# Kernel optimization log

Measured on AMD Instinct MI355X. Metric: run time of the kernel, lower is better.

The kernel has to match this reference:

```python
import jax, jax.numpy as jnp
import numpy as np
import math

IN_DIM = 1024
L = 4096
D_MODEL = 512
D_INNER = 1024   # expand=2 * d_model
D_STATE = 16
D_CONV = 4
DT_RANK = 32     # ceil(d_model / 16)
N_LAYERS = 2
RATE = 10


def setup_inputs() -> dict:
    key = jax.random.key(0)
    ks = iter(jax.random.split(key, 32))
    def w(shape, fan_in):
        return jax.random.normal(next(ks), shape, jnp.float32) * (1.0 / math.sqrt(fan_in))
    return {
        "x": jax.random.normal(next(ks), (1, L, IN_DIM), jnp.float32),
        "rate": RATE,
        "fc1_w": w((D_MODEL, IN_DIM), IN_DIM),
        "fc1_b": jnp.zeros((D_MODEL,), jnp.float32),
        "ln_w": jnp.ones((N_LAYERS, D_MODEL), jnp.float32),
        "ln_b": jnp.zeros((N_LAYERS, D_MODEL), jnp.float32),
        "in_proj_w": w((N_LAYERS, 2 * D_INNER, D_MODEL), D_MODEL),
        "conv_w": w((N_LAYERS, D_INNER, D_CONV), D_CONV),
        "conv_b": jnp.zeros((N_LAYERS, D_INNER), jnp.float32),
        "x_proj_w": w((N_LAYERS, DT_RANK + 2 * D_STATE, D_INNER), D_INNER),
        "dt_proj_w": w((N_LAYERS, D_INNER, DT_RANK), DT_RANK),
        "dt_proj_b": jax.random.normal(next(ks), (N_LAYERS, D_INNER), jnp.float32) * 0.1,
        "A_log": jnp.tile(jnp.log(jnp.arange(1, D_STATE + 1, dtype=jnp.float32)), (N_LAYERS, D_INNER, 1)),
        "D_skip": jnp.ones((N_LAYERS, D_INNER), jnp.float32),
        "out_proj_w": w((N_LAYERS, D_MODEL, D_INNER), D_INNER),
        "norm_w": jnp.ones((D_MODEL,), jnp.float32),
        "norm_b": jnp.zeros((D_MODEL,), jnp.float32),
        "attn_w1": w((128, D_MODEL), D_MODEL),
        "attn_b1": jnp.zeros((128,), jnp.float32),
        "attn_w2": w((1, 128), 128),
        "attn_b2": jnp.zeros((1,), jnp.float32),
        "out2048_w": w((2048, D_MODEL), D_MODEL),
        "out2048_b": jnp.zeros((2048,), jnp.float32),
    }


def _layernorm(x, w, b, eps=1e-5):
    mu = x.mean(-1, keepdims=True)
    var = ((x - mu) ** 2).mean(-1, keepdims=True)
    return (x - mu) * jax.lax.rsqrt(var + eps) * w + b


def _causal_conv(x, w, b):
    # depthwise causal conv: x [L, d], w [d, K] -> y[t, d] = sum_k w[d, k] * x[t - (K-1) + k, d]
    K = w.shape[1]
    xp = jnp.pad(x, ((K - 1, 0), (0, 0)))
    y = sum(xp[k:k + x.shape[0]] * w[:, k] for k in range(K))
    return y + b


def _selective_scan(u, dt, A, B, C, Dp, z):
    # u, dt, z: [L, d]; A: [d, n]; B, C: [L, n]; Dp: [d]
    def step(h, inp):
        dt_t, B_t, C_t, u_t = inp
        dA = jnp.exp(dt_t[:, None] * A)                    # [d, n]
        h = dA * h + (dt_t * u_t)[:, None] * B_t[None, :]  # [d, n]
        return h, h @ C_t                                  # y_t: [d]
    h0 = jnp.zeros((u.shape[1], A.shape[1]), u.dtype)
    _, y = jax.lax.scan(step, h0, (dt, B, C, u))
    return (y + u * Dp) * jax.nn.silu(z)


def _srmamba(h, perm, inv, in_w, cw, cb, xw, dtw, dtb, A_log, Dp, ow):
    xz = h @ in_w.T                         # [L, 2*d_inner]
    x, z = jnp.split(xz, 2, axis=-1)
    x, z = x[perm], z[perm]                 # sequence reordering (stride `rate`)
    x = jax.nn.silu(_causal_conv(x, cw, cb))
    dbl = x @ xw.T                          # [L, dt_rank + 2n]
    dt = jax.nn.softplus(dbl[:, :DT_RANK] @ dtw.T + dtb)
    B = dbl[:, DT_RANK:DT_RANK + D_STATE]
    C = dbl[:, DT_RANK + D_STATE:]
    y = _selective_scan(x, dt, -jnp.exp(A_log), B, C, Dp, z)
    return y[inv] @ ow.T                    # restore original order, out_proj


def reference(x, rate, fc1_w, fc1_b, ln_w, ln_b, in_proj_w, conv_w, conv_b, x_proj_w, dt_proj_w, dt_proj_b, A_log, D_skip, out_proj_w, norm_w, norm_b, attn_w1, attn_b1, attn_w2, attn_b2, out2048_w, out2048_b):
    h = jax.nn.relu(x[0] @ fc1_w.T + fc1_b)   # [L, 512]
    Lx = h.shape[0]
    perm = jnp.concatenate([jnp.arange(i, Lx, rate) for i in range(rate)])
    inv = jnp.argsort(perm)
    for l in range(N_LAYERS):
        h = h + _srmamba(_layernorm(h, ln_w[l], ln_b[l]), perm, inv,
                         in_proj_w[l], conv_w[l], conv_b[l], x_proj_w[l],
                         dt_proj_w[l], dt_proj_b[l], A_log[l], D_skip[l], out_proj_w[l])
    h = _layernorm(h, norm_w, norm_b)
    a = jnp.tanh(h @ attn_w1.T + attn_b1) @ attn_w2.T + attn_b2  # [L, 1]
    Aatt = jax.nn.softmax(a[:, 0])                                # [L]
    pooled = Aatt @ h                                             # [512]
    out = pooled @ out2048_w.T + out2048_b                        # [2048]
    return out[None, :], Aatt[None, None, :]
```

## Files before the change

### kernel.cpp

```cpp
#include <hip/hip_runtime.h>
#include <hip/hip_fp16.h>
#include <math.h>

#define L 4096
#define DIN 1024
#define DM 512
#define DI 1024
#define DS 16
#define DTR 32
#define NCH 128
#define CHK 32

typedef _Float16 v8h __attribute__((ext_vector_type(8)));
typedef float v4f __attribute__((ext_vector_type(4)));

__global__ void perm_k(int* __restrict__ perm, const int* __restrict__ ratep) {
    int p = blockIdx.x * blockDim.x + threadIdx.x;
    if (p >= L) return;
    int rate = ratep[0];
    int cum = 0;
    for (int g = 0; g < rate; ++g) {
        int sz = (L - g + rate - 1) / rate;
        if (p < cum + sz) { perm[p] = g + rate * (p - cum); return; }
        cum += sz;
    }
}

__global__ __launch_bounds__(256) void f2h_multi_k(
    const float* __restrict__ s0, _Float16* __restrict__ d0, int b0,
    const float* __restrict__ s1, _Float16* __restrict__ d1, int b1,
    const float* __restrict__ s2, _Float16* __restrict__ d2, int b2,
    const float* __restrict__ s3, _Float16* __restrict__ d3, int b3)
{
    int b = blockIdx.x;
    const float* src; _Float16* dst; int lb;
    if (b < b0)                { src = s0; dst = d0; lb = b; }
    else if (b < b0 + b1)      { src = s1; dst = d1; lb = b - b0; }
    else if (b < b0 + b1 + b2) { src = s2; dst = d2; lb = b - b0 - b1; }
    else                       { src = s3; dst = d3; lb = b - b0 - b1 - b2; }
    int i = (lb * 256 + threadIdx.x) * 4;
    float4 v = *(const float4*)(src + i);
    _Float16 h4[4] = {(_Float16)v.x, (_Float16)v.y, (_Float16)v.z, (_Float16)v.w};
    *(uint2*)(dst + i) = *(uint2*)h4;
}

template<int ACT, int BNT, int HALF>
__global__ __launch_bounds__(256) void hgemm_nt(
    const _Float16* __restrict__ A, int lda,
    const _Float16* __restrict__ B, int ldb,
    void* __restrict__ Cv, int ldc,
    const float* __restrict__ bias, int K, int accum)
{
    constexpr int MI = (BNT == 128) ? 4 : 2;
    __shared__ _Float16 As[128][40];
    __shared__ _Float16 Bs[BNT][40];
    int tid = threadIdx.x;
    int m0 = blockIdx.y * 128, n0 = blockIdx.x * BNT;
    int lane = tid & 63, wave = tid >> 6;
    int wm, wn;
    if constexpr (BNT == 128) { wm = (wave >> 1) * 64; wn = (wave & 1) * 64; }
    else                      { wm = wave * 32;        wn = 0; }
    int quad = lane >> 4, r16 = lane & 15;
    v4f acc[MI][4] = {};

    int srow = tid >> 1;
    int scol = (tid & 1) * 16;
    const _Float16* Ag = A + (size_t)(m0 + srow) * lda + scol;
    int srowB = (BNT == 128) ? srow : (tid >> 2);
    int scolB = (BNT == 128) ? scol : (tid & 3) * 8;
    const _Float16* Bg = B + (size_t)(n0 + srowB) * ldb + scolB;

    uint4 a0, a1, b0, b1;
    a0 = *(const uint4*)(Ag);
    a1 = *(const uint4*)(Ag + 8);
    b0 = *(const uint4*)(Bg);
    if constexpr (BNT == 128) b1 = *(const uint4*)(Bg + 8);

    int KS = K / 32;
    for (int ks = 0; ks < KS; ++ks) {
        __syncthreads();
        *(uint4*)&As[srow][scol] = a0;
        *(uint4*)&As[srow][scol + 8] = a1;
        *(uint4*)&Bs[srowB][scolB] = b0;
        if constexpr (BNT == 128) *(uint4*)&Bs[srowB][scolB + 8] = b1;
        __syncthreads();
        if (ks + 1 < KS) {
            int k0 = (ks + 1) * 32;
            a0 = *(const uint4*)(Ag + k0);
            a1 = *(const uint4*)(Ag + k0 + 8);
            b0 = *(const uint4*)(Bg + k0);
            if constexpr (BNT == 128) b1 = *(const uint4*)(Bg + k0 + 8);
        }
        v8h af[MI], bf[4];
#pragma unroll
        for (int i = 0; i < MI; ++i)
            af[i] = *(const v8h*)&As[wm + i * 16 + r16][quad * 8];
#pragma unroll
        for (int j = 0; j < 4; ++j)
            bf[j] = *(const v8h*)&Bs[wn + j * 16 + r16][quad * 8];
#pragma unroll
        for (int i = 0; i < MI; ++i)
#pragma unroll
            for (int j = 0; j < 4; ++j)
                acc[i][j] = __builtin_amdgcn_mfma_f32_16x16x32_f16(
                    af[i], bf[j], acc[i][j], 0, 0, 0);
    }

#pragma unroll
    for (int i = 0; i < MI; ++i) {
#pragma unroll
        for (int j = 0; j < 4; ++j) {
            int col = n0 + wn + j * 16 + r16;
            int rbase = m0 + wm + i * 16 + quad * 4;
            float bv = bias ? bias[col] : 0.f;
#pragma unroll
            for (int r = 0; r < 4; ++r) {
                float v = acc[i][j][r] + bv;
                if (ACT == 1) v = fmaxf(v, 0.f);
                if constexpr (HALF) {
                    ((_Float16*)Cv)[(size_t)(rbase + r) * ldc + col] = (_Float16)v;
                } else {
                    float* p = (float*)Cv + (size_t)(rbase + r) * ldc + col;
                    if (accum) v += *p;
                    *p = v;
                }
            }
        }
    }
}

#define BM 64
#define BN 64
#define BKK 32
template<int ACT>
__global__ __launch_bounds__(256) void gemm_nt(
    const float* __restrict__ A, int lda,
    const float* __restrict__ B, int ldb,
    float* __restrict__ C, int ldc,
    const float* __restrict__ bias,
    int M, int N, int K, int kchunk, int accum,
    const float* __restrict__ w2, float* __restrict__ avec)
{
    __shared__ float As[BKK][BM + 4];
    __shared__ float Bs[BKK][BN + 4];
    int tid = threadIdx.x;
    int m0 = blockIdx.y * BM;
    int n0 = blockIdx.x * BN;
    int tx = tid & 15, ty = tid >> 4;
    float acc[4][4] = {};
    int arow = tid >> 3;
    int ak = (tid & 7) * 4;
    int kb = blockIdx.z * kchunk;
    int ke = min(K, kb + kchunk);

    for (int k0 = kb; k0 < ke; k0 += BKK) {
#pragma unroll
        for (int r = 0; r < 2; ++r) {
            int row = arow + r * 32;
            float4 va = *(const float4*)(A + (size_t)(m0 + row) * lda + k0 + ak);
            As[ak + 0][row] = va.x; As[ak + 1][row] = va.y;
            As[ak + 2][row] = va.z; As[ak + 3][row] = va.w;
            float4 vb = *(const float4*)(B + (size_t)(n0 + row) * ldb + k0 + ak);
            Bs[ak + 0][row] = vb.x; Bs[ak + 1][row] = vb.y;
            Bs[ak + 2][row] = vb.z; Bs[ak + 3][row] = vb.w;
        }
        __syncthreads();
#pragma unroll
        for (int kk = 0; kk < BKK; ++kk) {
            float4 a4 = *(const float4*)&As[kk][ty * 4];
            float4 b4 = *(const float4*)&Bs[kk][tx * 4];
            float a[4] = {a4.x, a4.y, a4.z, a4.w};
            float b[4] = {b4.x, b4.y, b4.z, b4.w};
#pragma unroll
            for (int i = 0; i < 4; ++i)
#pragma unroll
                for (int j = 0; j < 4; ++j)
                    acc[i][j] = fmaf(a[i], b[j], acc[i][j]);
        }
        __syncthreads();
    }

#pragma unroll
    for (int i = 0; i < 4; ++i) {
        int row = m0 + ty * 4 + i;
        int col = n0 + tx * 4;
        if (ACT == 4) {
            float part = 0.f;
#pragma unroll
            for (int j = 0; j < 4; ++j) {
                float xv = tanhf(acc[i][j] + bias[col + j]);
                part = fmaf(xv, w2[col + j], part);
            }
            atomicAdd(&avec[row], part);
            continue;
        }
        float* cp = C + (size_t)row * ldc + col;
        if (accum == 2) {
#pragma unroll
            for (int j = 0; j < 4; ++j) atomicAdd(cp + j, acc[i][j]);
            continue;
        }
#pragma unroll
        for (int j = 0; j < 4; ++j)
            cp[j] = acc[i][j] + (bias ? bias[col + j] : 0.f);
    }
}

__global__ __launch_bounds__(256) void layernorm_k(
    const float* __restrict__ x, const float* __restrict__ w,
    const float* __restrict__ b, float* __restrict__ o,
    _Float16* __restrict__ oh, float* __restrict__ avec,
    const float* __restrict__ b2)
{
    int row = blockIdx.x;
    int tid = threadIdx.x;
    const float* xr = x + (size_t)row * DM;
    float v0 = xr[tid], v1 = xr[tid + 256];
    float s = v0 + v1, ss = v0 * v0 + v1 * v1;
    for (int off = 32; off; off >>= 1) {
        s += __shfl_down(s, off, 64);
        ss += __shfl_down(ss, off, 64);
    }
    __shared__ float sm[4], sm2[4];
    int wave = tid >> 6, lane = tid & 63;
    if (lane == 0) { sm[wave] = s; sm2[wave] = ss; }
    __syncthreads();
    float tot = sm[0] + sm[1] + sm[2] + sm[3];
    float tot2 = sm2[0] + sm2[1] + sm2[2] + sm2[3];
    float mu = tot * (1.f / DM);
    float var = tot2 * (1.f / DM) - mu * mu;
    float rs = rsqrtf(var + 1e-5f);
    float y0 = (v0 - mu) * rs * w[tid] + b[tid];
    float y1 = (v1 - mu) * rs * w[tid + 256] + b[tid + 256];
    o[(size_t)row * DM + tid] = y0;
    o[(size_t)row * DM + tid + 256] = y1;
    if (oh) {
        oh[(size_t)row * DM + tid] = (_Float16)y0;
        oh[(size_t)row * DM + tid + 256] = (_Float16)y1;
    }
    if (avec && tid == 0) avec[row] = b2[0];
}

__global__ __launch_bounds__(256) void conv_silu_k(
    const _Float16* __restrict__ xz, const int* __restrict__ perm,
    const float* __restrict__ cw, const float* __restrict__ cb,
    float* __restrict__ xc, float* __restrict__ dbl)
{
    if (blockIdx.x < 256) {
        int zi = (blockIdx.x * 256 + threadIdx.x) * 4;
        *(float4*)(dbl + zi) = make_float4(0.f, 0.f, 0.f, 0.f);
    }
    int g = blockIdx.x * 256 + threadIdx.x;
    int c = g & (DI - 1), p = g >> 10;
    float acc = cb[c];
#pragma unroll
    for (int k = 0; k < 4; ++k) {
        int q = p + k - 3;
        if (q >= 0)
            acc = fmaf((float)xz[(size_t)perm[q] * (2 * DI) + c], cw[c * 4 + k], acc);
    }
    float sig = 1.f / (1.f + __expf(-acc));
    xc[g] = acc * sig;
}

__device__ __forceinline__ float dt_of(
    const float* __restrict__ dblrow, const v4f* __restrict__ dw, float dtbc)
{
    float dot = dtbc;
#pragma unroll
    for (int q = 0; q < 8; ++q) {
        v4f dr = *(const v4f*)(dblrow + q * 4);
#pragma unroll
        for (int r = 0; r < 4; ++r) dot = fmaf(dr[r], dw[q][r], dot);
    }
    return (dot > 20.f) ? dot : log1pf(__expf(dot));
}

__global__ __launch_bounds__(256) void scan_pass1(
    const float* __restrict__ u, const float* __restrict__ dbl,
    const float* __restrict__ dtw, const float* __restrict__ dtb,
    const float* __restrict__ A_log,
    float* __restrict__ Aprod, float* __restrict__ carry)
{
    int c = blockIdx.x * 256 + threadIdx.x;
    int j = blockIdx.y;
    float Ac[16];
#pragma unroll
    for (int s = 0; s < 16; ++s) Ac[s] = -__expf(A_log[c * DS + s]);
    v4f dw[8];
#pragma unroll
    for (int q = 0; q < 8; ++q) dw[q] = *(const v4f*)(dtw + c * DTR + q * 4);
    float dtbc = dtb[c];
    float ap[16], h[16];
#pragma unroll
    for (int s = 0; s < 16; ++s) { ap[s] = 1.f; h[s] = 0.f; }
    int t0 = j * CHK;
    for (int tt = 0; tt < CHK; ++tt) {
        int t = t0 + tt;
        const float* dblrow = dbl + (size_t)t * 64;
        float dtv = dt_of(dblrow, dw, dtbc);
        float uv  = u[(size_t)t * DI + c];
        v4f Bv[4];
#pragma unroll
        for (int q = 0; q < 4; ++q)
            Bv[q] = *(const v4f*)(dblrow + DTR + q * 4);
        float du = dtv * uv;
#pragma unroll
        for (int s = 0; s < 16; ++s) {
            float dA = __expf(dtv * Ac[s]);
            h[s] = fmaf(dA, h[s], du * Bv[s >> 2][s & 3]);
            ap[s] *= dA;
        }
    }
    size_t base = ((size_t)j * DI + c) * DS;
#pragma unroll
    for (int q = 0; q < 4; ++q) {
        *(v4f*)(Aprod + base + q * 4) = *(v4f*)&ap[q * 4];
        *(v4f*)(carry + base + q * 4) = *(v4f*)&h[q * 4];
    }
}

__global__ __launch_bounds__(256) void scan_pass2(
    const float* __restrict__ Aprod, const float* __restrict__ carry,
    float* __restrict__ Hin)
{
    int idx = blockIdx.x * 256 + threadIdx.x;
    float H = 0.f;
    Hin[idx] = 0.f;
    for (int j = 1; j < NCH; ++j) {
        H = fmaf(Aprod[(size_t)(j - 1) * (DI * DS) + idx], H,
                 carry[(size_t)(j - 1) * (DI * DS) + idx]);
        Hin[(size_t)j * (DI * DS) + idx] = H;
    }
}

__global__ __launch_bounds__(256) void scan_pass3(
    const float* __restrict__ u, const float* __restrict__ dbl,
    const float* __restrict__ dtw, const float* __restrict__ dtb,
    const _Float16* __restrict__ xz, const float* __restrict__ A_log,
    const float* __restrict__ Dsk, const int* __restrict__ perm,
    const float* __restrict__ Hin, _Float16* __restrict__ yo)
{
    int c = blockIdx.x * 256 + threadIdx.x;
    int j = blockIdx.y;
    float Ac[16];
#pragma unroll
    for (int s = 0; s < 16; ++s) Ac[s] = -__expf(A_log[c * DS + s]);
    v4f dw[8];
#pragma unroll
    for (int q = 0; q < 8; ++q) dw[q] = *(const v4f*)(dtw + c * DTR + q * 4);
    float dtbc = dtb[c];
    float Dp = Dsk[c];
    float h[16];
    size_t hbase = ((size_t)j * DI + c) * DS;
#pragma unroll
    for (int q = 0; q < 4; ++q)
        *(v4f*)&h[q * 4] = *(const v4f*)(Hin + hbase + q * 4);
    int t0 = j * CHK;
    for (int tt = 0; tt < CHK; ++tt) {
        int t = t0 + tt;
        const float* dblrow = dbl + (size_t)t * 64;
        float dtv = dt_of(dblrow, dw, dtbc);
        float uv  = u[(size_t)t * DI + c];
        v4f Bv[4], Cv[4];
#pragma unroll
        for (int q = 0; q < 4; ++q) {
            Bv[q] = *(const v4f*)(dblrow + DTR + q * 4);
            Cv[q] = *(const v4f*)(dblrow + DTR + DS + q * 4);
        }
        float du = dtv * uv;
        float y = 0.f;
#pragma unroll
        for (int s = 0; s < 16; ++s) {
            float dA = __expf(dtv * Ac[s]);
            h[s] = fmaf(dA, h[s], du * Bv[s >> 2][s & 3]);
            y = fmaf(h[s], Cv[s >> 2][s & 3], y);
        }
        int tp = perm[t];
        float z = (float)xz[(size_t)tp * (2 * DI) + DI + c];
        float sig = 1.f / (1.f + __expf(-z));
        yo[(size_t)tp * DI + c] = (_Float16)((y + uv * Dp) * (z * sig));
    }
}

__global__ __launch_bounds__(1024) void softmax_k(
    const float* __restrict__ a, float* __restrict__ out,
    float* __restrict__ pooled)
{
    int tid = threadIdx.x;
    if (tid < DM) pooled[tid] = 0.f;
    float v[4];
    float mx = -1e30f;
#pragma unroll
    for (int i = 0; i < 4; ++i) { v[i] = a[tid + i * 1024]; mx = fmaxf(mx, v[i]); }
    __shared__ float sm[16];
    for (int off = 32; off; off >>= 1) mx = fmaxf(mx, __shfl_xor(mx, off, 64));
    int wave = tid >> 6, lane = tid & 63;
    if (lane == 0) sm[wave] = mx;
    __syncthreads();
    if (tid < 16) {
        float m = sm[tid];
        for (int off = 8; off; off >>= 1) m = fmaxf(m, __shfl_xor(m, off, 64));
        sm[tid] = m;
    }
    __syncthreads();
    mx = sm[0];
    float s = 0.f;
#pragma unroll
    for (int i = 0; i < 4; ++i) { v[i] = __expf(v[i] - mx); s += v[i]; }
    for (int off = 32; off; off >>= 1) s += __shfl_xor(s, off, 64);
    __syncthreads();
    if (lane == 0) sm[wave] = s;
    __syncthreads();
    if (tid < 16) {
        float t2 = sm[tid];
        for (int off = 8; off; off >>= 1) t2 += __shfl_xor(t2, off, 64);
        sm[tid] = t2;
    }
    __syncthreads();
    float inv = 1.f / sm[0];
#pragma unroll
    for (int i = 0; i < 4; ++i) out[tid + i * 1024] = v[i] * inv;
}

__global__ __launch_bounds__(512) void pool_k(
    const float* __restrict__ aatt, const float* __restrict__ h,
    float* __restrict__ pooled)
{
    int m = threadIdx.x;
    int t0 = blockIdx.x * 128;
    float acc = 0.f;
    for (int r = 0; r < 128; ++r) {
        int t = t0 + r;
        acc = fmaf(aatt[t], h[(size_t)t * DM + m], acc);
    }
    atomicAdd(&pooled[m], acc);
}

__global__ __launch_bounds__(64) void out2048_k(
    const float* __restrict__ pooled, const float* __restrict__ w,
    const float* __restrict__ b, float* __restrict__ out)
{
    int n = blockIdx.x;
    int lane = threadIdx.x;
    const float* wr = w + (size_t)n * DM;
    float acc = 0.f;
#pragma unroll
    for (int k = 0; k < 8; ++k)
        acc = fmaf(wr[lane + k * 64], pooled[lane + k * 64], acc);
    for (int off = 32; off; off >>= 1) acc += __shfl_xor(acc, off, 64);
    if (lane == 0) out[n] = acc + b[n];
}

extern "C" void kernel_launch(void* const* d_in, const int* in_sizes, int n_in,
                              void* d_out, int out_size, void* d_ws, size_t ws_size,
                              hipStream_t stream) {
    const float* x     = (const float*)d_in[0];
    const int*   rate  = (const int*)d_in[1];
    const float* fc1_w = (const float*)d_in[2];
    const float* fc1_b = (const float*)d_in[3];
    const float* ln_w  = (const float*)d_in[4];
    const float* ln_b  = (const float*)d_in[5];
    const float* ipw   = (const float*)d_in[6];
    const float* cw    = (const float*)d_in[7];
    const float* cb    = (const float*)d_in[8];
    const float* xpw   = (const float*)d_in[9];
    const float* dtw   = (const float*)d_in[10];
    const float* dtpb  = (const float*)d_in[11];
    const float* A_log = (const float*)d_in[12];
    const float* Dsk   = (const float*)d_in[13];
    const float* opw   = (const float*)d_in[14];
    const float* nw    = (const float*)d_in[15];
    const float* nb    = (const float*)d_in[16];
    const float* aw1   = (const float*)d_in[17];
    const float* ab1   = (const float*)d_in[18];
    const float* aw2   = (const float*)d_in[19];
    const float* ab2   = (const float*)d_in[20];
    const float* ow    = (const float*)d_in[21];
    const float* ob    = (const float*)d_in[22];
    float* out = (float*)d_out;

    int* perm = (int*)d_ws;
    float* f = (float*)d_ws + 4096;
    float* h    = f; f += (size_t)L * DM;
    float* hln  = f; f += (size_t)L * DM;
    float* xc   = f; f += (size_t)L * DI;
    float* dbl  = f; f += (size_t)L * 64;
    float* avec = f; f += L;
    float* pooled = f; f += DM;
    float* Aprod = f; f += (size_t)NCH * DI * DS;
    float* carry = f; f += (size_t)NCH * DI * DS;
    float* Hin   = f; f += (size_t)NCH * DI * DS;
    _Float16* fh = (_Float16*)f;
    _Float16* xh     = fh; fh += (size_t)L * DIN;
    _Float16* hln_h  = fh; fh += (size_t)L * DM;
    _Float16* yo_h   = fh; fh += (size_t)L * DI;
    _Float16* xz_h   = fh; fh += (size_t)L * 2 * DI;
    _Float16* fc1w_h = fh; fh += (size_t)DM * DIN;
    _Float16* ipw_h  = fh; fh += (size_t)2 * 2 * DI * DM;
    _Float16* opw_h  = fh; fh += (size_t)2 * DM * DI;

    perm_k<<<16, 256, 0, stream>>>(perm, rate);

    f2h_multi_k<<<(L * DIN + DM * DIN + 2 * 2 * DI * DM + 2 * DM * DI) / 1024,
                  256, 0, stream>>>(
        x, xh, L * DIN / 1024,
        fc1_w, fc1w_h, DM * DIN / 1024,
        ipw, ipw_h, 2 * 2 * DI * DM / 1024,
        opw, opw_h, 2 * DM * DI / 1024);

    hgemm_nt<1, 64, 0><<<dim3(DM / 64, L / 128), 256, 0, stream>>>(
        xh, DIN, fc1w_h, DIN, h, DM, fc1_b, DIN, 0);

    for (int l = 0; l < 2; ++l) {
        layernorm_k<<<L, 256, 0, stream>>>(h, ln_w + l * DM, ln_b + l * DM,
                                           hln, hln_h, nullptr, nullptr);
        hgemm_nt<0, 128, 1><<<dim3(2 * DI / 128, L / 128), 256, 0, stream>>>(
            hln_h, DM, ipw_h + (size_t)l * 2 * DI * DM, DM, xz_h, 2 * DI,
            nullptr, DM, 0);
        conv_silu_k<<<L * DI / 256, 256, 0, stream>>>(
            xz_h, perm, cw + (size_t)l * DI * 4, cb + (size_t)l * DI, xc, dbl);
        gemm_nt<0><<<dim3(1, L / 64, 4), 256, 0, stream>>>(
            xc, DI, xpw + (size_t)l * 64 * DI, DI, dbl, 64, nullptr,
            L, 64, DI, DI / 4, 2, nullptr, nullptr);
        scan_pass1<<<dim3(DI / 256, NCH), 256, 0, stream>>>(
            xc, dbl, dtw + (size_t)l * DI * DTR, dtpb + (size_t)l * DI,
            A_log + (size_t)l * DI * DS, Aprod, carry);
        scan_pass2<<<DI * DS / 256, 256, 0, stream>>>(Aprod, carry, Hin);
        scan_pass3<<<dim3(DI / 256, NCH), 256, 0, stream>>>(
            xc, dbl, dtw + (size_t)l * DI * DTR, dtpb + (size_t)l * DI,
            xz_h, A_log + (size_t)l * DI * DS, Dsk + (size_t)l * DI,
            perm, Hin, yo_h);
        hgemm_nt<0, 64, 0><<<dim3(DM / 64, L / 128), 256, 0, stream>>>(
            yo_h, DI, opw_h + (size_t)l * DM * DI, DI, h, DM, nullptr, DI, 1);
    }

    layernorm_k<<<L, 256, 0, stream>>>(h, nw, nb, hln, nullptr, avec, ab2);
    gemm_nt<4><<<dim3(128 / 64, L / 64), 256, 0, stream>>>(
        hln, DM, aw1, DM, nullptr, 0, ab1, L, 128, DM, DM, 0, aw2, avec);
    softmax_k<<<1, 1024, 0, stream>>>(avec, out + 2048, pooled);
    pool_k<<<32, 512, 0, stream>>>(out + 2048, hln, pooled);
    out2048_k<<<2048, 64, 0, stream>>>(pooled, ow, ob, out);
}
```

Before: 620.0 us.

## Precompute dt via softplus GEMM and halve scan chunk length

Moves the dt_proj dot product and softplus out of both scan passes into a dedicated fp32 GEMM with a softplus epilogue, storing a full L x DI dt buffer. The scan passes then read dt directly instead of recomputing the 32-wide dot product twice per element. The scan chunking also changes from 128 chunks of 32 steps to 256 chunks of 16, raising parallelism in passes 1 and 3 but lengthening the serial pass 2 and doubling the Aprod/carry/Hin traffic. The extra dt buffer adds 16 MB of memory traffic per layer.

```diff
diff --git a/kernel.cpp b/kernel.cpp
--- a/kernel.cpp
+++ b/kernel.cpp
@@ -8,8 +8,8 @@
 #define DI 1024
 #define DS 16
 #define DTR 32
-#define NCH 128
-#define CHK 32
+#define NCH 256
+#define CHK 16
 
 typedef _Float16 v8h __attribute__((ext_vector_type(8)));
 typedef float v4f __attribute__((ext_vector_type(4)));
@@ -201,8 +201,11 @@
             continue;
         }
 #pragma unroll
-        for (int j = 0; j < 4; ++j)
-            cp[j] = acc[i][j] + (bias ? bias[col + j] : 0.f);
+        for (int j = 0; j < 4; ++j) {
+            float xv = acc[i][j] + (bias ? bias[col + j] : 0.f);
+            if (ACT == 2) xv = (xv > 20.f) ? xv : log1pf(__expf(xv));
+            cp[j] = xv;
+        }
     }
 }
 
@@ -263,23 +266,9 @@
     xc[g] = acc * sig;
 }
 
-__device__ __forceinline__ float dt_of(
-    const float* __restrict__ dblrow, const v4f* __restrict__ dw, float dtbc)
-{
-    float dot = dtbc;
-#pragma unroll
-    for (int q = 0; q < 8; ++q) {
-        v4f dr = *(const v4f*)(dblrow + q * 4);
-#pragma unroll
-        for (int r = 0; r < 4; ++r) dot = fmaf(dr[r], dw[q][r], dot);
-    }
-    return (dot > 20.f) ? dot : log1pf(__expf(dot));
-}
-
 __global__ __launch_bounds__(256) void scan_pass1(
-    const float* __restrict__ u, const float* __restrict__ dbl,
-    const float* __restrict__ dtw, const float* __restrict__ dtb,
-    const float* __restrict__ A_log,
+    const float* __restrict__ dt, const float* __restrict__ u,
+    const float* __restrict__ dbl, const float* __restrict__ A_log,
     float* __restrict__ Aprod, float* __restrict__ carry)
 {
     int c = blockIdx.x * 256 + threadIdx.x;
@@ -287,23 +276,18 @@
     float Ac[16];
 #pragma unroll
     for (int s = 0; s < 16; ++s) Ac[s] = -__expf(A_log[c * DS + s]);
-    v4f dw[8];
-#pragma unroll
-    for (int q = 0; q < 8; ++q) dw[q] = *(const v4f*)(dtw + c * DTR + q * 4);
-    float dtbc = dtb[c];
     float ap[16], h[16];
 #pragma unroll
     for (int s = 0; s < 16; ++s) { ap[s] = 1.f; h[s] = 0.f; }
     int t0 = j * CHK;
     for (int tt = 0; tt < CHK; ++tt) {
         int t = t0 + tt;
-        const float* dblrow = dbl + (size_t)t * 64;
-        float dtv = dt_of(dblrow, dw, dtbc);
+        float dtv = dt[(size_t)t * DI + c];
         float uv  = u[(size_t)t * DI + c];
         v4f Bv[4];
 #pragma unroll
         for (int q = 0; q < 4; ++q)
-            Bv[q] = *(const v4f*)(dblrow + DTR + q * 4);
+            Bv[q] = *(const v4f*)(dbl + (size_t)t * 64 + DTR + q * 4);
         float du = dtv * uv;
 #pragma unroll
         for (int s = 0; s < 16; ++s) {
@@ -335,21 +319,17 @@
 }
 
 __global__ __launch_bounds__(256) void scan_pass3(
-    const float* __restrict__ u, const float* __restrict__ dbl,
-    const float* __restrict__ dtw, const float* __restrict__ dtb,
-    const _Float16* __restrict__ xz, const float* __restrict__ A_log,
-    const float* __restrict__ Dsk, const int* __restrict__ perm,
-    const float* __restrict__ Hin, _Float16* __restrict__ yo)
+    const float* __restrict__ dt, const float* __restrict__ u,
+    const float* __restrict__ dbl, const _Float16* __restrict__ xz,
+    const float* __restrict__ A_log, const float* __restrict__ Dsk,
+    const int* __restrict__ perm, const float* __restrict__ Hin,
+    _Float16* __restrict__ yo)
 {
     int c = blockIdx.x * 256 + threadIdx.x;
     int j = blockIdx.y;
     float Ac[16];
 #pragma unroll
     for (int s = 0; s < 16; ++s) Ac[s] = -__expf(A_log[c * DS + s]);
-    v4f dw[8];
-#pragma unroll
-    for (int q = 0; q < 8; ++q) dw[q] = *(const v4f*)(dtw + c * DTR + q * 4);
-    float dtbc = dtb[c];
     float Dp = Dsk[c];
     float h[16];
     size_t hbase = ((size_t)j * DI + c) * DS;
@@ -359,14 +339,13 @@
     int t0 = j * CHK;
     for (int tt = 0; tt < CHK; ++tt) {
         int t = t0 + tt;
-        const float* dblrow = dbl + (size_t)t * 64;
-        float dtv = dt_of(dblrow, dw, dtbc);
+        float dtv = dt[(size_t)t * DI + c];
         float uv  = u[(size_t)t * DI + c];
         v4f Bv[4], Cv[4];
 #pragma unroll
         for (int q = 0; q < 4; ++q) {
-            Bv[q] = *(const v4f*)(dblrow + DTR + q * 4);
-            Cv[q] = *(const v4f*)(dblrow + DTR + DS + q * 4);
+            Bv[q] = *(const v4f*)(dbl + (size_t)t * 64 + DTR + q * 4);
+            Cv[q] = *(const v4f*)(dbl + (size_t)t * 64 + DTR + DS + q * 4);
         }
         float du = dtv * uv;
         float y = 0.f;
@@ -486,6 +465,7 @@
     float* hln  = f; f += (size_t)L * DM;
     float* xc   = f; f += (size_t)L * DI;
     float* dbl  = f; f += (size_t)L * 64;
+    float* dtv  = f; f += (size_t)L * DI;
     float* avec = f; f += L;
     float* pooled = f; f += DM;
     float* Aprod = f; f += (size_t)NCH * DI * DS;
@@ -523,14 +503,15 @@
         gemm_nt<0><<<dim3(1, L / 64, 4), 256, 0, stream>>>(
             xc, DI, xpw + (size_t)l * 64 * DI, DI, dbl, 64, nullptr,
             L, 64, DI, DI / 4, 2, nullptr, nullptr);
+        gemm_nt<2><<<dim3(DI / 64, L / 64), 256, 0, stream>>>(
+            dbl, 64, dtw + (size_t)l * DI * DTR, DTR, dtv, DI,
+            dtpb + (size_t)l * DI, L, DI, DTR, DTR, 0, nullptr, nullptr);
         scan_pass1<<<dim3(DI / 256, NCH), 256, 0, stream>>>(
-            xc, dbl, dtw + (size_t)l * DI * DTR, dtpb + (size_t)l * DI,
-            A_log + (size_t)l * DI * DS, Aprod, carry);
+            dtv, xc, dbl, A_log + (size_t)l * DI * DS, Aprod, carry);
         scan_pass2<<<DI * DS / 256, 256, 0, stream>>>(Aprod, carry, Hin);
         scan_pass3<<<dim3(DI / 256, NCH), 256, 0, stream>>>(
-            xc, dbl, dtw + (size_t)l * DI * DTR, dtpb + (size_t)l * DI,
-            xz_h, A_log + (size_t)l * DI * DS, Dsk + (size_t)l * DI,
-            perm, Hin, yo_h);
+            dtv, xc, dbl, xz_h, A_log + (size_t)l * DI * DS,
+            Dsk + (size_t)l * DI, perm, Hin, yo_h);
         hgemm_nt<0, 64, 0><<<dim3(DM / 64, L / 128), 256, 0, stream>>>(
             yo_h, DI, opw_h + (size_t)l * DM * DI, DI, h, DM, nullptr, DI, 1);
     }
```

Result: faster. 588.7 us (-5.0%).
